# Kernel tuning notes

Measured on AMD Instinct MI355X. Metric: run time of the kernel, lower is better.

The kernel has to match this reference:

```python
import jax, jax.numpy as jnp
import numpy as np

B, C, S, H = 8, 10, 512, 768
WIN = 5  # window_size


def setup_inputs() -> dict:
    key = jax.random.key(0)
    ks = jax.random.split(key, 12)
    def rn(k, shape, s=0.02):
        return jax.random.normal(k, shape, jnp.float32) * s
    return {
        "token_embeddings": jax.random.normal(ks[0], (B * C, S, H), jnp.float32),
        "w_tok": rn(ks[1], (1, H)), "b_tok": jnp.zeros((1,), jnp.float32),
        "w_sum": rn(ks[2], (H, H)), "b_sum": jnp.zeros((H,), jnp.float32),
        "w_proj": rn(ks[3], (2 * H, H)), "b_proj": jnp.zeros((2 * H,), jnp.float32),
        "w_ih_f": rn(ks[4], (4 * H, H)), "w_hh_f": rn(ks[5], (4 * H, H)),
        "b_ih_f": jnp.zeros((4 * H,), jnp.float32), "b_hh_f": jnp.zeros((4 * H,), jnp.float32),
        "w_ih_b": rn(ks[6], (4 * H, H)), "w_hh_b": rn(ks[7], (4 * H, H)),
        "b_ih_b": jnp.zeros((4 * H,), jnp.float32), "b_hh_b": jnp.zeros((4 * H,), jnp.float32),
        "w_cls": rn(ks[8], (1, 2 * H)), "b_cls": jnp.zeros((1,), jnp.float32),
        "num_chunks": C,
    }


def _lstm_dir(x, w_ih, w_hh, b_ih, b_hh, reverse):
    # x: [B, T, H]; PyTorch gate order i, f, g, o
    Bs, T, Hin = x.shape
    Hh = w_hh.shape[1]
    xs = jnp.einsum('bth,gh->btg', x, w_ih) + b_ih  # precompute input projections
    xs = jnp.swapaxes(xs, 0, 1)  # [T, B, 4H]
    if reverse:
        xs = xs[::-1]
    def step(carry, xt):
        h, c = carry
        g = xt + h @ w_hh.T + b_hh
        i, f, gg, o = jnp.split(g, 4, axis=-1)
        c = jax.nn.sigmoid(f) * c + jax.nn.sigmoid(i) * jnp.tanh(gg)
        h = jax.nn.sigmoid(o) * jnp.tanh(c)
        return (h, c), h
    init = (jnp.zeros((Bs, Hh), x.dtype), jnp.zeros((Bs, Hh), x.dtype))
    _, hs = jax.lax.scan(step, init, xs)
    if reverse:
        hs = hs[::-1]
    return jnp.swapaxes(hs, 0, 1)  # [B, T, Hh]


def reference(token_embeddings, w_tok, b_tok, w_sum, b_sum, w_proj, b_proj,
              w_ih_f, w_hh_f, b_ih_f, b_hh_f, w_ih_b, w_hh_b, b_ih_b, b_hh_b,
              w_cls, b_cls, num_chunks):
    BC, S_, H_ = token_embeddings.shape
    Bsz = BC // num_chunks
    # token_predictor + sigmoid -> [BC, S]
    scores = jax.nn.sigmoid(jnp.einsum('bsh,oh->bs', token_embeddings, w_tok) + b_tok[0])
    pad = WIN // 2
    padded = jnp.pad(scores, ((0, 0), (pad, pad)))
    cs = jnp.pad(jnp.cumsum(padded, axis=1), ((0, 0), (1, 0)))
    windowed = (cs[:, WIN:] - cs[:, :-WIN]) / WIN  # [BC, S]
    # summarize: score-weighted sum over tokens, then linear
    weighted = jnp.einsum('bsh,bs->bh', token_embeddings, windowed)
    summ = weighted @ w_sum.T + b_sum  # [BC, H]
    summ = summ.reshape(Bsz, num_chunks, H_).mean(axis=1)
    summ = summ @ w_proj.T + b_proj  # [B, 2H]
    # CLS-token embeddings per chunk -> biLSTM
    chunk = token_embeddings[:, 0, :].reshape(Bsz, num_chunks, H_)
    hf = _lstm_dir(chunk, w_ih_f, w_hh_f, b_ih_f, b_hh_f, False)
    hb = _lstm_dir(chunk, w_ih_b, w_hh_b, b_ih_b, b_hh_b, True)
    glob = jnp.concatenate([hf, hb], axis=-1)[:, -1, :]  # [B, 2H]
    combined = glob + summ
    class_probs = jax.nn.sigmoid(combined @ w_cls.T + b_cls)[:, 0]
    return (class_probs, windowed, summ)
```

## Files before the change

### kernel.cpp

```cpp
#include <hip/hip_runtime.h>

namespace {

constexpr int Bsz = 8, NC = 10, BC = 80, S = 512, H = 768, G4 = 3072, H2 = 1536;
constexpr int FA_CH = 64, FA_ROWS = 8, FA_STG = 12;
constexpr int FA_BLK = BC * FA_CH;
constexpr int XF_BLK = 960, XB_BLK = 96;
constexpr int XG_BLK = XF_BLK + XB_BLK;
constexpr int NBACK = 96;
constexpr int HP = 772;

typedef float f32x4 __attribute__((ext_vector_type(4)));

__device__ __forceinline__ float sigm(float x){ return 1.0f/(1.0f + __expf(-x)); }
__device__ __forceinline__ float tanh_fast(float x){ return 1.0f - 2.0f/(__expf(2.0f*x) + 1.0f); }
__device__ __forceinline__ float vdot(f32x4 a, f32x4 b){ f32x4 m = a*b; return m.x+m.y+m.z+m.w; }
__device__ __forceinline__ float wred(float v){
  #pragma unroll
  for (int m = 32; m; m >>= 1) v += __shfl_xor(v, m, 64);
  return v;
}

__device__ __forceinline__ void coh_load6(f32x4 (&d)[6],
    const f32x4* p0, const f32x4* p1, const f32x4* p2,
    const f32x4* p3, const f32x4* p4, const f32x4* p5){
  asm volatile(
    "global_load_dwordx4 %0, %6, off sc0 sc1\n\t"
    "global_load_dwordx4 %1, %7, off sc0 sc1\n\t"
    "global_load_dwordx4 %2, %8, off sc0 sc1\n\t"
    "global_load_dwordx4 %3, %9, off sc0 sc1\n\t"
    "global_load_dwordx4 %4, %10, off sc0 sc1\n\t"
    "global_load_dwordx4 %5, %11, off sc0 sc1\n\t"
    "s_waitcnt vmcnt(0)"
    : "=&v"(d[0]), "=&v"(d[1]), "=&v"(d[2]), "=&v"(d[3]), "=&v"(d[4]), "=&v"(d[5])
    : "v"(p0), "v"(p1), "v"(p2), "v"(p3), "v"(p4), "v"(p5)
    : "memory");
}
__device__ __forceinline__ void coh_store1(float* p, float v){
  asm volatile("global_store_dword %0, %1, off sc0 sc1" :: "v"(p), "v"(v) : "memory");
}

__global__ __launch_bounds__(256) void k_fa(
    const float* __restrict__ tok, const float* __restrict__ w_tok,
    const float* __restrict__ b_tok, float* __restrict__ win_out,
    float* __restrict__ wpart, unsigned* __restrict__ ctr){
  __shared__ float smemF[FA_STG * HP];
  __shared__ float scr[FA_STG];
  __shared__ float wsh[FA_ROWS];
  int blk = blockIdx.x, tid = threadIdx.x;

  if (blk == 0 && tid < 16) ctr[tid] = 0;

  int bc = blk >> 6, ch = blk & 63;
  int s0 = ch * FA_ROWS;
  #pragma unroll
  for (int i = 0; i < 9; i++){
    int f = i * 256 + tid;
    int row = f / 192, c4 = f % 192;
    int gs = s0 - 2 + row;
    if (gs >= 0 && gs < S)
      *(f32x4*)&smemF[row * HP + c4 * 4] =
        *(const f32x4*)&tok[((size_t)bc * S + gs) * H + c4 * 4];
  }
  __syncthreads();
  if (tid < 192){
    int r = tid >> 4, e = tid & 15;
    int gs = s0 - 2 + r;
    const f32x4* wq = (const f32x4*)w_tok;
    float acc = 0.f;
    #pragma unroll
    for (int i = 0; i < 12; i++){
      int k = e + 16 * i;
      acc += vdot(*(const f32x4*)&smemF[r * HP + k * 4], wq[k]);
    }
    acc += __shfl_xor(acc, 1, 64);
    acc += __shfl_xor(acc, 2, 64);
    acc += __shfl_xor(acc, 4, 64);
    acc += __shfl_xor(acc, 8, 64);
    if (e == 0) scr[r] = (gs >= 0 && gs < S) ? sigm(acc + b_tok[0]) : 0.f;
  }
  __syncthreads();
  if (tid < FA_ROWS){
    float w = (scr[tid] + scr[tid+1] + scr[tid+2] + scr[tid+3] + scr[tid+4]) * 0.2f;
    wsh[tid] = w;
    win_out[(size_t)bc * S + s0 + tid] = w;
  }
  __syncthreads();
  if (tid < 192){
    f32x4 acc = {0.f, 0.f, 0.f, 0.f};
    #pragma unroll
    for (int i = 0; i < FA_ROWS; i++){
      float w = wsh[i];
      f32x4 a = *(const f32x4*)&smemF[(i + 2) * HP + tid * 4];
      acc += a * w;
    }
    *(f32x4*)&wpart[((size_t)ch * BC + bc) * H + tid * 4] = acc;
  }
}

__global__ __launch_bounds__(256) void k_xg(
    const float* __restrict__ tok,
    const float* __restrict__ w_ih_f, const float* __restrict__ b_ih_f, const float* __restrict__ b_hh_f,
    const float* __restrict__ w_ih_b, const float* __restrict__ b_ih_b, const float* __restrict__ b_hh_b,
    float* __restrict__ xg, float* __restrict__ gbwd){
  __shared__ float smemX[8 * HP];
  int blk = blockIdx.x, tid = threadIdx.x;
  bool fwd = (blk < XF_BLK);
  int rblk, base_bc = 0;
  const float *w, *bi, *bh; float* outp;
  if (fwd){ rblk = blk / 10; base_bc = (blk % 10) * 8; w = w_ih_f; bi = b_ih_f; bh = b_hh_f; outp = xg; }
  else    { rblk = blk - XF_BLK;                      w = w_ih_b; bi = b_ih_b; bh = b_hh_b; outp = gbwd; }
  #pragma unroll
  for (int i = 0; i < 6; i++){
    int f = i * 256 + tid;
    int bl = f / 192, c4 = f % 192;
    size_t bc = fwd ? (size_t)(base_bc + bl) : ((size_t)bl * NC + NC - 1);
    *(f32x4*)&smemX[bl * HP + c4 * 4] = *(const f32x4*)&tok[bc * (size_t)S * H + c4 * 4];
  }
  __syncthreads();
  {
    int bl = tid & 7, rl = tid >> 3;
    int r = rblk * 32 + rl;
    const f32x4* wr = (const f32x4*)(w + (size_t)r * H);
    float acc = 0.f;
    #pragma unroll 8
    for (int k = 0; k < 192; k++)
      acc += vdot(*(const f32x4*)&smemX[bl * HP + k * 4], wr[k]);
    int ob = fwd ? (base_bc + bl) : bl;
    outp[(size_t)ob * G4 + r] = acc + bi[r] + bh[r];
  }
}

struct BackArgs {
  const float *w_sum, *b_sum, *w_proj, *b_proj;
  const float *w_hh, *xg, *gbwd, *w_cls, *b_cls, *wpart;
  float *wmean, *s1, *summ_out, *hx, *cls_out;
  unsigned *ctr;
};

__global__ __launch_bounds__(256) void k_back(BackArgs A){
  __shared__ float smem[12992];
  float* h_sh  = smem;
  float* a_sh  = smem + 6176;
  float* c_sh  = smem + 12352;
  float* g_sh  = smem + 12416;
  float* pg_sh = smem + 12672;
  int tid = threadIdx.x, lane = tid & 63, wv = tid >> 6, blkx = blockIdx.x;

  auto gbar = [&](int slot){
    asm volatile("s_waitcnt vmcnt(0)" ::: "memory");
    __syncthreads();
    if (tid == 0){
      __hip_atomic_fetch_add(&A.ctr[slot], 1u, __ATOMIC_RELAXED, __HIP_MEMORY_SCOPE_AGENT);
      while (__hip_atomic_load(&A.ctr[slot], __ATOMIC_RELAXED, __HIP_MEMORY_SCOPE_AGENT) < (unsigned)NBACK)
        __builtin_amdgcn_s_sleep(1);
    }
    __syncthreads();
  };

  auto stage6 = [&](float* dst, const float* src){
    const f32x4* s4 = (const f32x4*)src;
    f32x4 d[6];
    coh_load6(d, s4 + tid, s4 + 256 + tid, s4 + 512 + tid,
                 s4 + 768 + tid, s4 + 1024 + tid, s4 + 1280 + tid);
    #pragma unroll
    for (int i = 0; i < 6; i++){
      int f = i * 256 + tid, b = f / 192, j4 = f % 192;
      *(f32x4*)&dst[b * HP + j4 * 4] = d[i];
    }
  };

  auto do_step = [&](int t){
    int jl = tid >> 5, g = (tid >> 3) & 3, b = tid & 7;
    int j = blkx * 8 + jl;
    int r = g * H + j;
    const f32x4* wr = (const f32x4*)(A.w_hh + (size_t)r * H);
    float acc = 0.f;
    #pragma unroll 8
    for (int k = 0; k < 192; k++)
      acc += vdot(*(const f32x4*)&h_sh[b * HP + k * 4], wr[k]);
    g_sh[jl * 32 + g * 8 + b] = acc + A.xg[((size_t)b * NC + t) * G4 + r];
    __syncthreads();
    if (tid < 64){
      int jj = tid >> 3, b2 = tid & 7;
      float gi = g_sh[jj*32 + b2],      gf = g_sh[jj*32 + 8 + b2];
      float gg = g_sh[jj*32 + 16 + b2], go = g_sh[jj*32 + 24 + b2];
      float c = sigm(gf) * c_sh[tid] + sigm(gi) * tanh_fast(gg);
      c_sh[tid] = c;
      coh_store1(&A.hx[(t & 1) * (Bsz*H) + b2 * H + blkx * 8 + jj],
                 sigm(go) * tanh_fast(c));
    }
  };

  {
    int out = tid >> 2, ps = tid & 3;
    int idx = blkx * 64 + out;
    int b = idx / H, hh = idx % H;
    float acc = 0.f;
    for (int p = ps * 16; p < ps * 16 + 16; p++)
      #pragma unroll
      for (int c = 0; c < NC; c++)
        acc += A.wpart[((size_t)p * BC + b * NC + c) * H + hh];
    pg_sh[out * 5 + ps] = acc;
  }
  __syncthreads();
  if (tid < 64){
    float acc = pg_sh[tid*5] + pg_sh[tid*5+1] + pg_sh[tid*5+2] + pg_sh[tid*5+3];
    coh_store1(&A.wmean[blkx * 64 + tid], acc * 0.1f);
    int jl = tid >> 3, b2 = tid & 7, j = blkx * 8 + jl;
    const float* gp = A.xg + (size_t)(b2 * NC) * G4;
    float c = sigm(gp[j]) * tanh_fast(gp[2*H + j]);
    c_sh[tid] = c;
    coh_store1(&A.hx[b2 * H + j], sigm(gp[3*H + j]) * tanh_fast(c));
  }
  gbar(0);

  stage6(a_sh, A.wmean);
  stage6(h_sh, A.hx);
  __syncthreads();
  {
    int out = tid >> 2, q = tid & 3;
    int ol = out >> 3, b = out & 7;
    int o = blkx * 8 + ol;
    const f32x4* wq = (const f32x4*)(A.w_sum + (size_t)o * H) + q * 48;
    float acc = 0.f;
    #pragma unroll 8
    for (int k = 0; k < 48; k++)
      acc += vdot(*(const f32x4*)&a_sh[b * HP + (q * 48 + k) * 4], wq[k]);
    acc += __shfl_xor(acc, 1, 64);
    acc += __shfl_xor(acc, 2, 64);
    if (q == 0) coh_store1(&A.s1[(size_t)b * H + o], acc + A.b_sum[o]);
  }
  do_step(1);
  gbar(1);

  stage6(a_sh, A.s1);
  stage6(h_sh, A.hx + Bsz*H);
  __syncthreads();
  {
    int out = tid >> 1, hf = tid & 1;
    int ol = out >> 3, b = out & 7;
    int o = blkx * 16 + ol;
    const f32x4* wq = (const f32x4*)(A.w_proj + (size_t)o * H) + hf * 96;
    float acc = 0.f;
    #pragma unroll 8
    for (int k = 0; k < 96; k++)
      acc += vdot(*(const f32x4*)&a_sh[b * HP + (hf * 96 + k) * 4], wq[k]);
    acc += __shfl_xor(acc, 1, 64);
    if (hf == 0) coh_store1(&A.summ_out[(size_t)b * H2 + o], acc + A.b_proj[o]);
  }
  do_step(2);
  gbar(2);

  for (int t = 3; t <= 9; t++){
    stage6(h_sh, A.hx + ((t - 1) & 1) * (Bsz*H));
    __syncthreads();
    do_step(t);
    gbar(t);
  }

  if (blkx == 0){
    float* comb = smem;
    {
      f32x4 d[6];
      const f32x4* h4 = (const f32x4*)(A.hx + Bsz*H);
      coh_load6(d, h4 + tid, h4 + 256 + tid, h4 + 512 + tid,
                   h4 + 768 + tid, h4 + 1024 + tid, h4 + 1280 + tid);
      #pragma unroll
      for (int i = 0; i < 6; i++){
        int f = i * 256 + tid, b = f / 192, e = (f % 192) * 4;
        *(f32x4*)&comb[b * H2 + e] = d[i];
      }
      #pragma unroll
      for (int u = 0; u < 6; u++){
        int f = u * 256 + tid;
        int b = f / 192, e = (f % 192) * 4;
        f32x4 gi = *(const f32x4*)&A.gbwd[(size_t)b * G4 + e];
        f32x4 gg = *(const f32x4*)&A.gbwd[(size_t)b * G4 + 2*H + e];
        f32x4 go = *(const f32x4*)&A.gbwd[(size_t)b * G4 + 3*H + e];
        f32x4 hb;
        hb.x = sigm(go.x) * tanh_fast(sigm(gi.x) * tanh_fast(gg.x));
        hb.y = sigm(go.y) * tanh_fast(sigm(gi.y) * tanh_fast(gg.y));
        hb.z = sigm(go.z) * tanh_fast(sigm(gi.z) * tanh_fast(gg.z));
        hb.w = sigm(go.w) * tanh_fast(sigm(gi.w) * tanh_fast(gg.w));
        *(f32x4*)&comb[b * H2 + H + e] = hb;
      }
    }
    __syncthreads();
    {
      f32x4 d[6];
      const f32x4* s4 = (const f32x4*)A.summ_out;
      coh_load6(d, s4 + tid, s4 + 256 + tid, s4 + 512 + tid,
                   s4 + 768 + tid, s4 + 1024 + tid, s4 + 1280 + tid);
      #pragma unroll
      for (int i = 0; i < 6; i++) *(f32x4*)&comb[(i * 256 + tid) * 4] += d[i];
      coh_load6(d, s4 + 1536 + tid, s4 + 1792 + tid, s4 + 2048 + tid,
                   s4 + 2304 + tid, s4 + 2560 + tid, s4 + 2816 + tid);
      #pragma unroll
      for (int i = 0; i < 6; i++) *(f32x4*)&comb[(1536 + i * 256 + tid) * 4] += d[i];
    }
    __syncthreads();
    for (int b = wv; b < Bsz; b += 4){
      const f32x4* c4 = (const f32x4*)&comb[b * H2];
      const f32x4* wc = (const f32x4*)A.w_cls;
      float acc = 0.f;
      #pragma unroll
      for (int k = 0; k < 6; k++)
        acc += vdot(c4[lane + 64*k], wc[lane + 64*k]);
      acc = wred(acc);
      if (lane == 0) A.cls_out[b] = sigm(acc + A.b_cls[0]);
    }
  }
}

}

extern "C" void kernel_launch(void* const* d_in, const int* in_sizes, int n_in,
                              void* d_out, int out_size, void* d_ws, size_t ws_size,
                              hipStream_t stream) {
  const float* tok    = (const float*)d_in[0];
  const float* w_tok  = (const float*)d_in[1];
  const float* b_tok  = (const float*)d_in[2];
  const float* w_sum  = (const float*)d_in[3];
  const float* b_sum  = (const float*)d_in[4];
  const float* w_proj = (const float*)d_in[5];
  const float* b_proj = (const float*)d_in[6];
  const float* w_ih_f = (const float*)d_in[7];
  const float* w_hh_f = (const float*)d_in[8];
  const float* b_ih_f = (const float*)d_in[9];
  const float* b_hh_f = (const float*)d_in[10];
  const float* w_ih_b = (const float*)d_in[11];
  const float* b_ih_b = (const float*)d_in[13];
  const float* b_hh_b = (const float*)d_in[14];
  const float* w_cls  = (const float*)d_in[15];
  const float* b_cls  = (const float*)d_in[16];

  float* out      = (float*)d_out;
  float* cls_out  = out;
  float* win_out  = out + 8;
  float* summ_out = out + 8 + BC * S;

  float* ws     = (float*)d_ws;
  float* wpart  = ws;
  float* wmean  = wpart + (size_t)FA_CH * BC * H;
  float* s1     = wmean + Bsz * H;
  float* xg     = s1 + Bsz * H;
  float* gbwd   = xg + (size_t)BC * G4;
  float* hx     = gbwd + (size_t)Bsz * G4;
  unsigned* ctr = (unsigned*)(hx + 2 * Bsz * H);

  k_fa<<<FA_BLK, 256, 0, stream>>>(tok, w_tok, b_tok, win_out, wpart, ctr);
  k_xg<<<XG_BLK, 256, 0, stream>>>(tok, w_ih_f, b_ih_f, b_hh_f,
                                   w_ih_b, b_ih_b, b_hh_b, xg, gbwd);

  BackArgs ba;
  ba.w_sum = w_sum; ba.b_sum = b_sum; ba.w_proj = w_proj; ba.b_proj = b_proj;
  ba.w_hh = w_hh_f; ba.xg = xg; ba.gbwd = gbwd; ba.w_cls = w_cls; ba.b_cls = b_cls;
  ba.wpart = wpart; ba.wmean = wmean; ba.s1 = s1; ba.summ_out = summ_out;
  ba.hx = hx; ba.cls_out = cls_out; ba.ctr = ctr;

  void* params[] = { &ba };
  hipLaunchCooperativeKernel(reinterpret_cast<void*>(k_back),
                             dim3(NBACK), dim3(256), params, 0, stream);
}
```

Measured before the change: 203.0 us.

## Cache per-block LSTM recurrent weights in shared memory and vectorize dot-product accumulators

Each persistent block of the backward kernel now loads its 32 rows of w_hh into shared memory once at kernel start and reads them from LDS in every recurrent step, instead of re-reading them from global memory at each of the nine steps. Separately, every dot-product loop now keeps a 4-wide vector accumulator and does the horizontal sum once at the end, which shortens the serial add chain per iteration. The larger shared buffer (about 150 KB) reduces occupancy and adds an upfront weight-load phase before the first barrier. The xg load in the step is also hoisted ahead of the dot product.

```diff
diff --git a/kernel.cpp b/kernel.cpp
--- a/kernel.cpp
+++ b/kernel.cpp
@@ -15,6 +15,7 @@
 __device__ __forceinline__ float sigm(float x){ return 1.0f/(1.0f + __expf(-x)); }
 __device__ __forceinline__ float tanh_fast(float x){ return 1.0f - 2.0f/(__expf(2.0f*x) + 1.0f); }
 __device__ __forceinline__ float vdot(f32x4 a, f32x4 b){ f32x4 m = a*b; return m.x+m.y+m.z+m.w; }
+__device__ __forceinline__ float hsum(f32x4 a){ return (a.x+a.y)+(a.z+a.w); }
 __device__ __forceinline__ float wred(float v){
   #pragma unroll
   for (int m = 32; m; m >>= 1) v += __shfl_xor(v, m, 64);
@@ -67,12 +68,13 @@
     int r = tid >> 4, e = tid & 15;
     int gs = s0 - 2 + r;
     const f32x4* wq = (const f32x4*)w_tok;
-    float acc = 0.f;
+    f32x4 a4 = {0.f, 0.f, 0.f, 0.f};
     #pragma unroll
     for (int i = 0; i < 12; i++){
       int k = e + 16 * i;
-      acc += vdot(*(const f32x4*)&smemF[r * HP + k * 4], wq[k]);
-    }
+      a4 += *(const f32x4*)&smemF[r * HP + k * 4] * wq[k];
+    }
+    float acc = hsum(a4);
     acc += __shfl_xor(acc, 1, 64);
     acc += __shfl_xor(acc, 2, 64);
     acc += __shfl_xor(acc, 4, 64);
@@ -122,12 +124,12 @@
     int bl = tid & 7, rl = tid >> 3;
     int r = rblk * 32 + rl;
     const f32x4* wr = (const f32x4*)(w + (size_t)r * H);
-    float acc = 0.f;
+    f32x4 a4 = {0.f, 0.f, 0.f, 0.f};
     #pragma unroll 8
     for (int k = 0; k < 192; k++)
-      acc += vdot(*(const f32x4*)&smemX[bl * HP + k * 4], wr[k]);
+      a4 += *(const f32x4*)&smemX[bl * HP + k * 4] * wr[k];
     int ob = fwd ? (base_bc + bl) : bl;
-    outp[(size_t)ob * G4 + r] = acc + bi[r] + bh[r];
+    outp[(size_t)ob * G4 + r] = hsum(a4) + bi[r] + bh[r];
   }
 }
 
@@ -139,12 +141,13 @@
 };
 
 __global__ __launch_bounds__(256) void k_back(BackArgs A){
-  __shared__ float smem[12992];
-  float* h_sh  = smem;
-  float* a_sh  = smem + 6176;
-  float* c_sh  = smem + 12352;
-  float* g_sh  = smem + 12416;
-  float* pg_sh = smem + 12672;
+  __shared__ float smem[37696];
+  float* w_sh  = smem;
+  float* h_sh  = smem + 24704;
+  float* a_sh  = smem + 30880;
+  float* c_sh  = smem + 37056;
+  float* g_sh  = smem + 37120;
+  float* pg_sh = smem + 37376;
   int tid = threadIdx.x, lane = tid & 63, wv = tid >> 6, blkx = blockIdx.x;
 
   auto gbar = [&](int slot){
@@ -170,16 +173,27 @@
     }
   };
 
+  #pragma unroll
+  for (int i = 0; i < 24; i++){
+    int f = i * 256 + tid;
+    int lr = f / 192, k = f % 192;
+    int g = lr & 3, jl = lr >> 2;
+    int r = g * H + blkx * 8 + jl;
+    *(f32x4*)&w_sh[lr * HP + k * 4] = *(const f32x4*)&A.w_hh[(size_t)r * H + k * 4];
+  }
+
   auto do_step = [&](int t){
-    int jl = tid >> 5, g = (tid >> 3) & 3, b = tid & 7;
-    int j = blkx * 8 + jl;
-    int r = g * H + j;
-    const f32x4* wr = (const f32x4*)(A.w_hh + (size_t)r * H);
-    float acc = 0.f;
+    int b = tid & 7, lr = tid >> 3;
+    int g = lr & 3, jl = lr >> 2;
+    int r = g * H + blkx * 8 + jl;
+    float xgv = A.xg[((size_t)b * NC + t) * G4 + r];
+    const f32x4* wr = (const f32x4*)&w_sh[lr * HP];
+    const f32x4* hb = (const f32x4*)&h_sh[b * HP];
+    f32x4 a4 = {0.f, 0.f, 0.f, 0.f};
     #pragma unroll 8
     for (int k = 0; k < 192; k++)
-      acc += vdot(*(const f32x4*)&h_sh[b * HP + k * 4], wr[k]);
-    g_sh[jl * 32 + g * 8 + b] = acc + A.xg[((size_t)b * NC + t) * G4 + r];
+      a4 += wr[k] * hb[k];
+    g_sh[jl * 32 + g * 8 + b] = hsum(a4) + xgv;
     __syncthreads();
     if (tid < 64){
       int jj = tid >> 3, b2 = tid & 7;
@@ -223,10 +237,11 @@
     int ol = out >> 3, b = out & 7;
     int o = blkx * 8 + ol;
     const f32x4* wq = (const f32x4*)(A.w_sum + (size_t)o * H) + q * 48;
-    float acc = 0.f;
+    f32x4 a4 = {0.f, 0.f, 0.f, 0.f};
     #pragma unroll 8
     for (int k = 0; k < 48; k++)
-      acc += vdot(*(const f32x4*)&a_sh[b * HP + (q * 48 + k) * 4], wq[k]);
+      a4 += *(const f32x4*)&a_sh[b * HP + (q * 48 + k) * 4] * wq[k];
+    float acc = hsum(a4);
     acc += __shfl_xor(acc, 1, 64);
     acc += __shfl_xor(acc, 2, 64);
     if (q == 0) coh_store1(&A.s1[(size_t)b * H + o], acc + A.b_sum[o]);
@@ -242,10 +257,11 @@
     int ol = out >> 3, b = out & 7;
     int o = blkx * 16 + ol;
     const f32x4* wq = (const f32x4*)(A.w_proj + (size_t)o * H) + hf * 96;
-    float acc = 0.f;
+    f32x4 a4 = {0.f, 0.f, 0.f, 0.f};
     #pragma unroll 8
     for (int k = 0; k < 96; k++)
-      acc += vdot(*(const f32x4*)&a_sh[b * HP + (hf * 96 + k) * 4], wq[k]);
+      a4 += *(const f32x4*)&a_sh[b * HP + (hf * 96 + k) * 4] * wq[k];
+    float acc = hsum(a4);
     acc += __shfl_xor(acc, 1, 64);
     if (hf == 0) coh_store1(&A.summ_out[(size_t)b * H2 + o], acc + A.b_proj[o]);
   }
@@ -303,11 +319,11 @@
     for (int b = wv; b < Bsz; b += 4){
       const f32x4* c4 = (const f32x4*)&comb[b * H2];
       const f32x4* wc = (const f32x4*)A.w_cls;
-      float acc = 0.f;
+      f32x4 a4 = {0.f, 0.f, 0.f, 0.f};
       #pragma unroll
       for (int k = 0; k < 6; k++)
-        acc += vdot(c4[lane + 64*k], wc[lane + 64*k]);
-      acc = wred(acc);
+        a4 += c4[lane + 64*k] * wc[lane + 64*k];
+      float acc = wred(hsum(a4));
       if (lane == 0) A.cls_out[b] = sigm(acc + A.b_cls[0]);
     }
   }
```

Measured after the change: 185.1 us. 1.1x faster.
